# Optimization experiments

Measured on AMD Instinct MI355X. Metric: run time of the kernel, lower is better.

Reference implementation:

```python
import jax, jax.numpy as jnp
import numpy as np

N = 100000
E = 1000000
D_IN = 64
H1, C1 = 12, 12   # conv1: heads=12, out=12 -> concat 144
H2, C2 = 1, 64    # conv2: heads=1, out=64
NEG_SLOPE = 0.2
ALPHA = 0.5       # SSGConv alpha, K=1


def setup_inputs() -> dict:
    key = jax.random.key(0)
    ks = jax.random.split(key, 16)
    features = jax.random.normal(ks[0], (N, D_IN), dtype=jnp.float32)
    # edges with no self loops (PyG GATv2 removes then re-adds self loops)
    src = jax.random.randint(ks[1], (E,), 0, N)
    off = jax.random.randint(ks[2], (E,), 1, N)
    dst = (src + off) % N
    edge_index = jnp.stack([src, dst]).astype(jnp.int64)
    g = lambda k, shape, fan: (jax.random.normal(k, shape, jnp.float32) * (1.0 / np.sqrt(fan)))
    params = dict(
        W_ssg=g(ks[3], (D_IN, D_IN), D_IN), b_ssg=jnp.zeros((D_IN,), jnp.float32),
        W1l=g(ks[4], (D_IN, H1 * C1), D_IN), b1l=jnp.zeros((H1 * C1,), jnp.float32),
        W1r=g(ks[5], (D_IN, H1 * C1), D_IN), b1r=jnp.zeros((H1 * C1,), jnp.float32),
        att1=g(ks[6], (H1, C1), C1), bias1=jnp.zeros((H1 * C1,), jnp.float32),
        W2l=g(ks[7], (H1 * C1, H2 * C2), H1 * C1), b2l=jnp.zeros((H2 * C2,), jnp.float32),
        W2r=g(ks[8], (H1 * C1, H2 * C2), H1 * C1), b2r=jnp.zeros((H2 * C2,), jnp.float32),
        att2=g(ks[9], (H2, C2), C2), bias2=jnp.zeros((H2 * C2,), jnp.float32),
    )
    return dict(features=features, edge_index=edge_index, **params)


def _add_self_loops(src, dst):
    loop = jnp.arange(N, dtype=src.dtype)
    return jnp.concatenate([src, loop]), jnp.concatenate([dst, loop])


def _ssg_conv(x, src, dst, W, b):
    # gcn_norm with self loops, edge weight 1
    s, d = _add_self_loops(src, dst)
    deg = jax.ops.segment_sum(jnp.ones_like(s, dtype=x.dtype), d, num_segments=N)
    dinv = jnp.where(deg > 0, jax.lax.rsqrt(deg), 0.0)
    norm = dinv[s] * dinv[d]                      # [E+N]
    agg = jax.ops.segment_sum(x[s] * norm[:, None], d, num_segments=N)
    h = ALPHA * x + (1.0 - ALPHA) * agg           # K=1
    return h @ W + b


def _gatv2_conv(x, src, dst, Wl, bl, Wr, br, att, bias, Hh, Cc):
    s, d = _add_self_loops(src, dst)
    xl = (x @ Wl + bl).reshape(N, Hh, Cc)
    xr = (x @ Wr + br).reshape(N, Hh, Cc)
    e = jax.nn.leaky_relu(xl[s] + xr[d], NEG_SLOPE)       # [E', H, C]
    logits = jnp.einsum('ehc,hc->eh', e, att)             # [E', H]
    m = jax.ops.segment_max(logits, d, num_segments=N)    # [N, H]
    a = jnp.exp(logits - m[d])
    denom = jax.ops.segment_sum(a, d, num_segments=N)
    a = a / (denom[d] + 1e-16)                            # segment softmax
    out = jax.ops.segment_sum(xl[s] * a[:, :, None], d, num_segments=N)
    return out.reshape(N, Hh * Cc) + bias


def reference(features, edge_index, W_ssg, b_ssg, W1l, b1l, W1r, b1r,
              att1, bias1, W2l, b2l, W2r, b2r, att2, bias2):
    src, dst = edge_index[0], edge_index[1]
    x = _ssg_conv(features, src, dst, W_ssg, b_ssg)
    x = _gatv2_conv(x, src, dst, W1l, b1l, W1r, b1r, att1, bias1, H1, C1)
    x = _gatv2_conv(x, src, dst, W2l, b2l, W2r, b2r, att2, bias2, H2, C2)
    return x
```

## Files before the change

kernel.cpp:

```cpp
#include <hip/hip_runtime.h>

#define NNODE 100000
#define NEDGE 1000000
#define CAP 64

typedef __attribute__((ext_vector_type(4))) float f32x4;
typedef __attribute__((ext_vector_type(8))) short bf16x8;

__device__ __forceinline__ float lrelu(float x){ return x >= 0.f ? x : 0.2f*x; }
__device__ __forceinline__ unsigned short f2bf(float f){
    unsigned u = __float_as_uint(f);
    unsigned r = (u + 0x7FFFu + ((u >> 16) & 1u)) >> 16;
    return (unsigned short)r;
}
__device__ __forceinline__ float bf2f(unsigned short h){
    return __uint_as_float(((unsigned)h) << 16);
}

__global__ void detect_kernel(const int* __restrict__ ei, int* __restrict__ flag){
    if (threadIdx.x == 0 && blockIdx.x == 0){
        int nz = 0;
        for (int i = 1; i < 64; i += 2) nz |= ei[i];
        flag[0] = (nz == 0) ? 1 : 0;
    }
}

__global__ __launch_bounds__(256) void scatter_kernel(const int* __restrict__ ei,
                                                      const int* __restrict__ flag,
                                                      int* __restrict__ cnt,
                                                      int* __restrict__ col){
    int e = blockIdx.x * 256 + threadIdx.x;
    if (e >= NEDGE) return;
    int s, d;
    if (flag[0]){ s = ei[2*e]; d = ei[2*(NEDGE + e)]; }
    else        { s = ei[e];   d = ei[NEDGE + e]; }
    if ((unsigned)s < NNODE && (unsigned)d < NNODE){
        int p = atomicAdd(&cnt[d], 1);
        if (p < CAP) col[d*CAP + p] = s;
    }
}

__global__ __launch_bounds__(256) void dinv_kernel(const int* __restrict__ cnt,
                                                   float* __restrict__ dinv){
    int i = blockIdx.x * 256 + threadIdx.x;
    if (i < NNODE) dinv[i] = rsqrtf((float)(cnt[i] + 1));
}

__global__ __launch_bounds__(256) void foldw_kernel(const float* __restrict__ Wssg,
                                                    const float* __restrict__ bssg,
                                                    const float* __restrict__ W1l,
                                                    const float* __restrict__ b1l,
                                                    const float* __restrict__ W1r,
                                                    const float* __restrict__ b1r,
                                                    unsigned short* __restrict__ Wct,
                                                    float* __restrict__ bc){
    int id = blockIdx.x * 256 + threadIdx.x;
    if (id < 2*64*144){
        int which = id / (64*144);
        int rem = id - which*64*144;
        int k = rem / 144, j = rem - (rem/144)*144;
        const float* W1 = which ? W1r : W1l;
        float s = 0.f;
        #pragma unroll 8
        for (int c = 0; c < 64; ++c)
            s = fmaf(Wssg[k*64 + c], W1[c*144 + j], s);
        Wct[(size_t)(which*144 + j)*64 + k] = f2bf(s);
    }
    if (id < 2*144){
        int which = id / 144, j = id - which*144;
        const float* W1 = which ? W1r : W1l;
        const float* b1 = which ? b1r : b1l;
        float s = b1[j];
        #pragma unroll 8
        for (int c = 0; c < 64; ++c)
            s = fmaf(bssg[c], W1[c*144 + j], s);
        bc[which*144 + j] = s;
    }
}

__global__ __launch_bounds__(256) void castw2_kernel(const float* __restrict__ W2l,
                                                     const float* __restrict__ b2l,
                                                     const float* __restrict__ W2r,
                                                     const float* __restrict__ b2r,
                                                     unsigned short* __restrict__ W2t,
                                                     float* __restrict__ b2c){
    int id = blockIdx.x * 256 + threadIdx.x;
    if (id < 128*160){
        int j = id / 160, k = id - (id/160)*160;
        float v = 0.f;
        if (k < 144) v = (j < 64) ? W2l[k*64 + j] : W2r[k*64 + (j - 64)];
        W2t[(size_t)j*160 + k] = f2bf(v);
    }
    if (id < 128) b2c[id] = (id < 64) ? b2l[id] : b2r[id - 64];
}

__global__ __launch_bounds__(256) void ssg_kernel(const float* __restrict__ x,
                                                  const int* __restrict__ col,
                                                  const int* __restrict__ cnt,
                                                  const float* __restrict__ dinv,
                                                  unsigned short* __restrict__ hb){
    int wid = threadIdx.x >> 6, lane = threadIdx.x & 63;
    int d = blockIdx.x * 4 + wid;
    int cq = lane & 15, eq = lane >> 4;
    float di = dinv[d];
    int deg = min(cnt[d], CAP);
    int myc = (lane < deg) ? col[d*CAP + lane] : 0;
    float wl = (lane < deg) ? dinv[myc] : 0.f;
    float a0 = 0.f, a1 = 0.f, a2 = 0.f, a3 = 0.f;
    for (int e0 = 0; e0 < deg; e0 += 4){
        int e = e0 + eq;
        bool val = e < deg;
        int idx = val ? e : 0;
        int se = __shfl(myc, idx);
        float w = __shfl(wl, idx);
        if (!val) w = 0.f;
        float4 v = *(const float4*)&x[(size_t)se*64 + 4*cq];
        a0 = fmaf(w, v.x, a0);
        a1 = fmaf(w, v.y, a1);
        a2 = fmaf(w, v.z, a2);
        a3 = fmaf(w, v.w, a3);
    }
    #pragma unroll
    for (int m = 16; m < 64; m <<= 1){
        a0 += __shfl_xor(a0, m);
        a1 += __shfl_xor(a1, m);
        a2 += __shfl_xor(a2, m);
        a3 += __shfl_xor(a3, m);
    }
    if (eq == 0){
        float4 xd = *(const float4*)&x[(size_t)d*64 + 4*cq];
        float dd = di*di;
        ushort4 o;
        o.x = f2bf(0.5f*xd.x + 0.5f*fmaf(di, a0, dd*xd.x));
        o.y = f2bf(0.5f*xd.y + 0.5f*fmaf(di, a1, dd*xd.y));
        o.z = f2bf(0.5f*xd.z + 0.5f*fmaf(di, a2, dd*xd.z));
        o.w = f2bf(0.5f*xd.w + 0.5f*fmaf(di, a3, dd*xd.w));
        *(ushort4*)&hb[(size_t)d*64 + 4*cq] = o;
    }
}

template<int K, int OUT1, int OUT2>
__global__ __launch_bounds__(256) void gemm_mfma_kernel(const unsigned short* __restrict__ Xb,
                                                        const unsigned short* __restrict__ Wt,
                                                        const float* __restrict__ Bc,
                                                        unsigned short* __restrict__ Y1,
                                                        unsigned short* __restrict__ Y2){
    constexpr int OUT = OUT1 + OUT2;
    constexpr int NT = OUT / 16;
    int wid = threadIdx.x >> 6, lane = threadIdx.x & 63;
    int m = lane & 15, kg = lane >> 4;
    int row0 = blockIdx.x * 64 + wid * 16;
    int rA = row0 + m; if (rA > NNODE-1) rA = NNODE-1;
    f32x4 acc[NT];
    #pragma unroll
    for (int t = 0; t < NT; ++t) acc[t] = (f32x4){0.f, 0.f, 0.f, 0.f};
    #pragma unroll
    for (int k0 = 0; k0 < K; k0 += 32){
        bf16x8 a = *(const bf16x8*)&Xb[(size_t)rA*K + k0 + 8*kg];
        #pragma unroll
        for (int t = 0; t < NT; ++t){
            bf16x8 b = *(const bf16x8*)&Wt[(size_t)(t*16 + m)*K + k0 + 8*kg];
            acc[t] = __builtin_amdgcn_mfma_f32_16x16x32_bf16(a, b, acc[t], 0, 0, 0);
        }
    }
    int rbase = row0 + 4*kg;
    #pragma unroll
    for (int t = 0; t < NT; ++t){
        int colg = t*16 + m;
        float bias = Bc[colg];
        #pragma unroll
        for (int r = 0; r < 4; ++r){
            int gr = rbase + r;
            if (gr < NNODE){
                unsigned short v = f2bf(acc[t][r] + bias);
                if (colg < OUT1) Y1[(size_t)gr*OUT1 + colg] = v;
                else             Y2[(size_t)gr*OUT2 + (colg - OUT1)] = v;
            }
        }
    }
}

__global__ __launch_bounds__(192) void gat1_kernel(const unsigned short* __restrict__ xl,
                                                   const unsigned short* __restrict__ xr,
                                                   const int* __restrict__ col,
                                                   const int* __restrict__ cnt,
                                                   const float* __restrict__ att,
                                                   const float* __restrict__ bias,
                                                   unsigned short* __restrict__ xg){
    __shared__ __align__(16) float V[16][148];
    __shared__ float A[16][13];
    __shared__ int scol[65];
    int d = blockIdx.x, t = threadIdx.x;
    int deg = min(cnt[d], CAP);
    int ne = deg + 1;
    if (t < deg) scol[t] = col[d*CAP + t];
    if (t == deg) scol[t] = d;
    int h = t % 12;
    int eslot = t / 12;
    float xrr[12], attr[12];
    {
        const ushort4* xrp = (const ushort4*)&xr[(size_t)d*144 + h*12];
        ushort4 q0 = xrp[0], q1 = xrp[1], q2 = xrp[2];
        xrr[0]=bf2f(q0.x); xrr[1]=bf2f(q0.y); xrr[2]=bf2f(q0.z); xrr[3]=bf2f(q0.w);
        xrr[4]=bf2f(q1.x); xrr[5]=bf2f(q1.y); xrr[6]=bf2f(q1.z); xrr[7]=bf2f(q1.w);
        xrr[8]=bf2f(q2.x); xrr[9]=bf2f(q2.y); xrr[10]=bf2f(q2.z); xrr[11]=bf2f(q2.w);
    }
    #pragma unroll
    for (int c = 0; c < 12; ++c) attr[c] = att[h*12 + c];
    int hh = t / 12;
    float acc = 0.f, l = 0.f;
    __syncthreads();
    for (int e0 = 0; e0 < ne; e0 += 16){
        int e = e0 + eslot;
        if (e < ne){
            const ushort4* row = (const ushort4*)&xl[(size_t)scol[e]*144 + h*12];
            ushort4 q0 = row[0], q1 = row[1], q2 = row[2];
            float v0=bf2f(q0.x), v1=bf2f(q0.y), v2=bf2f(q0.z), v3=bf2f(q0.w);
            float v4=bf2f(q1.x), v5=bf2f(q1.y), v6=bf2f(q1.z), v7=bf2f(q1.w);
            float v8=bf2f(q2.x), v9=bf2f(q2.y), v10=bf2f(q2.z), v11=bf2f(q2.w);
            float s = 0.f;
            s = fmaf(lrelu(v0 + xrr[0]),  attr[0],  s);
            s = fmaf(lrelu(v1 + xrr[1]),  attr[1],  s);
            s = fmaf(lrelu(v2 + xrr[2]),  attr[2],  s);
            s = fmaf(lrelu(v3 + xrr[3]),  attr[3],  s);
            s = fmaf(lrelu(v4 + xrr[4]),  attr[4],  s);
            s = fmaf(lrelu(v5 + xrr[5]),  attr[5],  s);
            s = fmaf(lrelu(v6 + xrr[6]),  attr[6],  s);
            s = fmaf(lrelu(v7 + xrr[7]),  attr[7],  s);
            s = fmaf(lrelu(v8 + xrr[8]),  attr[8],  s);
            s = fmaf(lrelu(v9 + xrr[9]),  attr[9],  s);
            s = fmaf(lrelu(v10 + xrr[10]), attr[10], s);
            s = fmaf(lrelu(v11 + xrr[11]), attr[11], s);
            A[eslot][h] = __expf(s);
            float4 f0 = make_float4(v0, v1, v2, v3);
            float4 f1 = make_float4(v4, v5, v6, v7);
            float4 f2 = make_float4(v8, v9, v10, v11);
            *(float4*)&V[eslot][h*12]     = f0;
            *(float4*)&V[eslot][h*12 + 4] = f1;
            *(float4*)&V[eslot][h*12 + 8] = f2;
        }
        __syncthreads();
        if (t < 144){
            int lim = ne - e0; if (lim > 16) lim = 16;
            for (int ee = 0; ee < lim; ++ee){
                float a  = A[ee][hh];
                float xv = V[ee][t];
                l += a;
                acc = fmaf(a, xv, acc);
            }
        }
        __syncthreads();
    }
    if (t < 144) xg[(size_t)d*160 + t] = f2bf(acc / (l + 1e-16f) + bias[t]);
    else if (t < 160) xg[(size_t)d*160 + t] = 0;
}

__global__ __launch_bounds__(256) void gat2_kernel(const unsigned short* __restrict__ xl,
                                                   const unsigned short* __restrict__ xr,
                                                   const int* __restrict__ col,
                                                   const int* __restrict__ cnt,
                                                   const float* __restrict__ att,
                                                   const float* __restrict__ bias,
                                                   float* __restrict__ out){
    __shared__ float V[4][8][68];
    __shared__ float Aw[4][8];
    int wid = threadIdx.x >> 6, lane = threadIdx.x & 63;
    int d0 = blockIdx.x * 4;
    int d = d0 + wid;
    int deg = min(cnt[d], 63);
    int ne = deg + 1;
    int nemax = 1;
    #pragma unroll
    for (int j = 0; j < 4; ++j) nemax = max(nemax, min(cnt[d0+j], 63) + 1);
    int eq = lane >> 3, cq = lane & 7;
    float4 xra, xrb;
    {
        ushort4 u0 = *(const ushort4*)&xr[(size_t)d*64 + 8*cq];
        ushort4 u1 = *(const ushort4*)&xr[(size_t)d*64 + 8*cq + 4];
        xra = make_float4(bf2f(u0.x), bf2f(u0.y), bf2f(u0.z), bf2f(u0.w));
        xrb = make_float4(bf2f(u1.x), bf2f(u1.y), bf2f(u1.z), bf2f(u1.w));
    }
    float4 ata = *(const float4*)&att[8*cq];
    float4 atb = *(const float4*)&att[8*cq + 4];
    int myc = (lane < deg) ? col[d*CAP + lane] : d;
    float acc = 0.f, l = 0.f;
    for (int e0 = 0; e0 < nemax; e0 += 8){
        int e = e0 + eq;
        bool val = (e < ne);
        int se = __shfl(myc, val ? e : 0);
        float4 va = make_float4(0.f,0.f,0.f,0.f), vb = va;
        if (val){
            ushort4 u0 = *(const ushort4*)&xl[(size_t)se*64 + 8*cq];
            ushort4 u1 = *(const ushort4*)&xl[(size_t)se*64 + 8*cq + 4];
            va = make_float4(bf2f(u0.x), bf2f(u0.y), bf2f(u0.z), bf2f(u0.w));
            vb = make_float4(bf2f(u1.x), bf2f(u1.y), bf2f(u1.z), bf2f(u1.w));
        }
        float part = 0.f;
        part = fmaf(lrelu(va.x + xra.x), ata.x, part);
        part = fmaf(lrelu(va.y + xra.y), ata.y, part);
        part = fmaf(lrelu(va.z + xra.z), ata.z, part);
        part = fmaf(lrelu(va.w + xra.w), ata.w, part);
        part = fmaf(lrelu(vb.x + xrb.x), atb.x, part);
        part = fmaf(lrelu(vb.y + xrb.y), atb.y, part);
        part = fmaf(lrelu(vb.z + xrb.z), atb.z, part);
        part = fmaf(lrelu(vb.w + xrb.w), atb.w, part);
        part += __shfl_xor(part, 1);
        part += __shfl_xor(part, 2);
        part += __shfl_xor(part, 4);
        *(float4*)&V[wid][eq][8*cq]     = va;
        *(float4*)&V[wid][eq][8*cq + 4] = vb;
        if (cq == 0) Aw[wid][eq] = val ? __expf(part) : 0.f;
        __syncthreads();
        int lim = ne - e0; if (lim > 8) lim = 8;
        for (int j = 0; j < lim; ++j){
            float a = Aw[wid][j];
            l += a;
            acc = fmaf(a, V[wid][j][lane], acc);
        }
        __syncthreads();
    }
    out[(size_t)d*64 + lane] = acc / (l + 1e-16f) + bias[lane];
}

extern "C" void kernel_launch(void* const* d_in, const int* in_sizes, int n_in,
                              void* d_out, int out_size, void* d_ws, size_t ws_size,
                              hipStream_t stream){
    const float* feat  = (const float*)d_in[0];
    const int*   ei    = (const int*)d_in[1];
    const float* W_ssg = (const float*)d_in[2];
    const float* b_ssg = (const float*)d_in[3];
    const float* W1l   = (const float*)d_in[4];
    const float* b1l   = (const float*)d_in[5];
    const float* W1r   = (const float*)d_in[6];
    const float* b1r   = (const float*)d_in[7];
    const float* att1  = (const float*)d_in[8];
    const float* bias1 = (const float*)d_in[9];
    const float* W2l   = (const float*)d_in[10];
    const float* b2l   = (const float*)d_in[11];
    const float* W2r   = (const float*)d_in[12];
    const float* b2r   = (const float*)d_in[13];
    const float* att2  = (const float*)d_in[14];
    const float* bias2 = (const float*)d_in[15];
    float* out = (float*)d_out;

    char* ws = (char*)d_ws;
    size_t off = 0;
    auto alloc = [&](size_t bytes)->void*{
        void* p = ws + off; off = (off + bytes + 255) & ~(size_t)255; return p;
    };
    int*            flag = (int*)           alloc(4);
    int*            cnt  = (int*)           alloc((size_t)NNODE*4);
    int*            col  = (int*)           alloc((size_t)NNODE*CAP*4);
    float*          dinv = (float*)         alloc((size_t)NNODE*4);
    unsigned short* hb   = (unsigned short*)alloc((size_t)NNODE*64*2);
    unsigned short* xl1b = (unsigned short*)alloc((size_t)NNODE*144*2);
    unsigned short* xr1b = (unsigned short*)alloc((size_t)NNODE*144*2);
    unsigned short* xg   = (unsigned short*)alloc((size_t)NNODE*160*2);
    unsigned short* xl2b = (unsigned short*)alloc((size_t)NNODE*64*2);
    unsigned short* xr2b = (unsigned short*)alloc((size_t)NNODE*64*2);
    unsigned short* Wct  = (unsigned short*)alloc((size_t)288*64*2);
    float*          bc   = (float*)         alloc((size_t)288*4);
    unsigned short* W2t  = (unsigned short*)alloc((size_t)128*160*2);
    float*          b2c  = (float*)         alloc((size_t)128*4);

    hipMemsetAsync(cnt, 0, (size_t)NNODE*4, stream);
    detect_kernel<<<1, 64, 0, stream>>>(ei, flag);
    scatter_kernel<<<(NEDGE + 255)/256, 256, 0, stream>>>(ei, flag, cnt, col);
    dinv_kernel<<<(NNODE + 255)/256, 256, 0, stream>>>(cnt, dinv);
    foldw_kernel<<<72, 256, 0, stream>>>(W_ssg, b_ssg, W1l, b1l, W1r, b1r, Wct, bc);
    castw2_kernel<<<80, 256, 0, stream>>>(W2l, b2l, W2r, b2r, W2t, b2c);

    ssg_kernel<<<NNODE/4, 256, 0, stream>>>(feat, col, cnt, dinv, hb);

    gemm_mfma_kernel<64,144,144><<<1563, 256, 0, stream>>>(hb, Wct, bc, xl1b, xr1b);

    gat1_kernel<<<NNODE, 192, 0, stream>>>(xl1b, xr1b, col, cnt, att1, bias1, xg);

    gemm_mfma_kernel<160,64,64><<<1563, 256, 0, stream>>>(xg, W2t, b2c, xl2b, xr2b);

    gat2_kernel<<<NNODE/4, 256, 0, stream>>>(xl2b, xr2b, col, cnt, att2, bias2, out);
}
```

Baseline: 493.5 us.

## Merge setup kernels, widen ssg loads, and vectorize gat1 aggregation

Combines the dinv, weight-fold and W2 cast kernels into a single launch to cut launch overhead, and turns the flag detection into one parallel ballot. The ssg kernel now gives each lane 8 channels with two float4 loads, so 8 edges are processed per wavefront step. The gat1 aggregation splits edges across 4 groups, with float4 channel reads from shared memory, and adds a cross-group reduction through shared memory. These trade extra shared memory and a sync for more parallel accumulation and fewer launches.

```diff
diff --git a/kernel.cpp b/kernel.cpp
--- a/kernel.cpp
+++ b/kernel.cpp
@@ -18,11 +18,10 @@
 }
 
 __global__ void detect_kernel(const int* __restrict__ ei, int* __restrict__ flag){
-    if (threadIdx.x == 0 && blockIdx.x == 0){
-        int nz = 0;
-        for (int i = 1; i < 64; i += 2) nz |= ei[i];
-        flag[0] = (nz == 0) ? 1 : 0;
-    }
+    int t = threadIdx.x;
+    int nz = ei[2*t + 1];
+    unsigned long long b = __ballot(nz != 0);
+    if (t == 0) flag[0] = (b == 0ULL) ? 1 : 0;
 }
 
 __global__ __launch_bounds__(256) void scatter_kernel(const int* __restrict__ ei,
@@ -40,58 +39,59 @@
     }
 }
 
-__global__ __launch_bounds__(256) void dinv_kernel(const int* __restrict__ cnt,
-                                                   float* __restrict__ dinv){
-    int i = blockIdx.x * 256 + threadIdx.x;
-    if (i < NNODE) dinv[i] = rsqrtf((float)(cnt[i] + 1));
-}
-
-__global__ __launch_bounds__(256) void foldw_kernel(const float* __restrict__ Wssg,
+__global__ __launch_bounds__(256) void setup_kernel(const int* __restrict__ cnt,
+                                                    float* __restrict__ dinv,
+                                                    const float* __restrict__ Wssg,
                                                     const float* __restrict__ bssg,
                                                     const float* __restrict__ W1l,
                                                     const float* __restrict__ b1l,
                                                     const float* __restrict__ W1r,
                                                     const float* __restrict__ b1r,
                                                     unsigned short* __restrict__ Wct,
-                                                    float* __restrict__ bc){
-    int id = blockIdx.x * 256 + threadIdx.x;
-    if (id < 2*64*144){
-        int which = id / (64*144);
-        int rem = id - which*64*144;
-        int k = rem / 144, j = rem - (rem/144)*144;
-        const float* W1 = which ? W1r : W1l;
-        float s = 0.f;
-        #pragma unroll 8
-        for (int c = 0; c < 64; ++c)
-            s = fmaf(Wssg[k*64 + c], W1[c*144 + j], s);
-        Wct[(size_t)(which*144 + j)*64 + k] = f2bf(s);
-    }
-    if (id < 2*144){
-        int which = id / 144, j = id - which*144;
-        const float* W1 = which ? W1r : W1l;
-        const float* b1 = which ? b1r : b1l;
-        float s = b1[j];
-        #pragma unroll 8
-        for (int c = 0; c < 64; ++c)
-            s = fmaf(bssg[c], W1[c*144 + j], s);
-        bc[which*144 + j] = s;
-    }
-}
-
-__global__ __launch_bounds__(256) void castw2_kernel(const float* __restrict__ W2l,
-                                                     const float* __restrict__ b2l,
-                                                     const float* __restrict__ W2r,
-                                                     const float* __restrict__ b2r,
-                                                     unsigned short* __restrict__ W2t,
-                                                     float* __restrict__ b2c){
-    int id = blockIdx.x * 256 + threadIdx.x;
-    if (id < 128*160){
-        int j = id / 160, k = id - (id/160)*160;
-        float v = 0.f;
-        if (k < 144) v = (j < 64) ? W2l[k*64 + j] : W2r[k*64 + (j - 64)];
-        W2t[(size_t)j*160 + k] = f2bf(v);
-    }
-    if (id < 128) b2c[id] = (id < 64) ? b2l[id] : b2r[id - 64];
+                                                    float* __restrict__ bc,
+                                                    const float* __restrict__ W2l,
+                                                    const float* __restrict__ b2l,
+                                                    const float* __restrict__ W2r,
+                                                    const float* __restrict__ b2r,
+                                                    unsigned short* __restrict__ W2t,
+                                                    float* __restrict__ b2c){
+    int b = blockIdx.x;
+    if (b < 391){
+        int i = b * 256 + threadIdx.x;
+        if (i < NNODE) dinv[i] = rsqrtf((float)(cnt[i] + 1));
+    } else if (b < 463){
+        int id = (b - 391) * 256 + threadIdx.x;
+        if (id < 2*64*144){
+            int which = id / (64*144);
+            int rem = id - which*64*144;
+            int k = rem / 144, j = rem - (rem/144)*144;
+            const float* W1 = which ? W1r : W1l;
+            float s = 0.f;
+            #pragma unroll 8
+            for (int c = 0; c < 64; ++c)
+                s = fmaf(Wssg[k*64 + c], W1[c*144 + j], s);
+            Wct[(size_t)(which*144 + j)*64 + k] = f2bf(s);
+        }
+        if (id < 2*144){
+            int which = id / 144, j = id - which*144;
+            const float* W1 = which ? W1r : W1l;
+            const float* b1 = which ? b1r : b1l;
+            float s = b1[j];
+            #pragma unroll 8
+            for (int c = 0; c < 64; ++c)
+                s = fmaf(bssg[c], W1[c*144 + j], s);
+            bc[which*144 + j] = s;
+        }
+    } else {
+        int id = (b - 463) * 256 + threadIdx.x;
+        if (id < 128*160){
+            int j = id / 160, k = id - (id/160)*160;
+            float v = 0.f;
+            if (k < 144) v = (j < 64) ? W2l[k*64 + j] : W2r[k*64 + (j - 64)];
+            W2t[(size_t)j*160 + k] = f2bf(v);
+        }
+        if (id < 128) b2c[id] = (id < 64) ? b2l[id] : b2r[id - 64];
+    }
 }
 
 __global__ __launch_bounds__(256) void ssg_kernel(const float* __restrict__ x,
@@ -101,41 +101,48 @@
                                                   unsigned short* __restrict__ hb){
     int wid = threadIdx.x >> 6, lane = threadIdx.x & 63;
     int d = blockIdx.x * 4 + wid;
-    int cq = lane & 15, eq = lane >> 4;
+    int cq = lane & 7, eq = lane >> 3;
     float di = dinv[d];
     int deg = min(cnt[d], CAP);
     int myc = (lane < deg) ? col[d*CAP + lane] : 0;
     float wl = (lane < deg) ? dinv[myc] : 0.f;
-    float a0 = 0.f, a1 = 0.f, a2 = 0.f, a3 = 0.f;
-    for (int e0 = 0; e0 < deg; e0 += 4){
+    float a0=0.f,a1=0.f,a2=0.f,a3=0.f,a4=0.f,a5=0.f,a6=0.f,a7=0.f;
+    for (int e0 = 0; e0 < deg; e0 += 8){
         int e = e0 + eq;
         bool val = e < deg;
         int idx = val ? e : 0;
         int se = __shfl(myc, idx);
         float w = __shfl(wl, idx);
         if (!val) w = 0.f;
-        float4 v = *(const float4*)&x[(size_t)se*64 + 4*cq];
-        a0 = fmaf(w, v.x, a0);
-        a1 = fmaf(w, v.y, a1);
-        a2 = fmaf(w, v.z, a2);
-        a3 = fmaf(w, v.w, a3);
-    }
-    #pragma unroll
-    for (int m = 16; m < 64; m <<= 1){
-        a0 += __shfl_xor(a0, m);
-        a1 += __shfl_xor(a1, m);
-        a2 += __shfl_xor(a2, m);
-        a3 += __shfl_xor(a3, m);
+        float4 v0 = *(const float4*)&x[(size_t)se*64 + 8*cq];
+        float4 v1 = *(const float4*)&x[(size_t)se*64 + 8*cq + 4];
+        a0 = fmaf(w, v0.x, a0); a1 = fmaf(w, v0.y, a1);
+        a2 = fmaf(w, v0.z, a2); a3 = fmaf(w, v0.w, a3);
+        a4 = fmaf(w, v1.x, a4); a5 = fmaf(w, v1.y, a5);
+        a6 = fmaf(w, v1.z, a6); a7 = fmaf(w, v1.w, a7);
+    }
+    #pragma unroll
+    for (int m = 8; m < 64; m <<= 1){
+        a0 += __shfl_xor(a0, m); a1 += __shfl_xor(a1, m);
+        a2 += __shfl_xor(a2, m); a3 += __shfl_xor(a3, m);
+        a4 += __shfl_xor(a4, m); a5 += __shfl_xor(a5, m);
+        a6 += __shfl_xor(a6, m); a7 += __shfl_xor(a7, m);
     }
     if (eq == 0){
-        float4 xd = *(const float4*)&x[(size_t)d*64 + 4*cq];
+        float4 xd0 = *(const float4*)&x[(size_t)d*64 + 8*cq];
+        float4 xd1 = *(const float4*)&x[(size_t)d*64 + 8*cq + 4];
         float dd = di*di;
-        ushort4 o;
-        o.x = f2bf(0.5f*xd.x + 0.5f*fmaf(di, a0, dd*xd.x));
-        o.y = f2bf(0.5f*xd.y + 0.5f*fmaf(di, a1, dd*xd.y));
-        o.z = f2bf(0.5f*xd.z + 0.5f*fmaf(di, a2, dd*xd.z));
-        o.w = f2bf(0.5f*xd.w + 0.5f*fmaf(di, a3, dd*xd.w));
-        *(ushort4*)&hb[(size_t)d*64 + 4*cq] = o;
+        ushort4 o0, o1;
+        o0.x = f2bf(0.5f*xd0.x + 0.5f*fmaf(di, a0, dd*xd0.x));
+        o0.y = f2bf(0.5f*xd0.y + 0.5f*fmaf(di, a1, dd*xd0.y));
+        o0.z = f2bf(0.5f*xd0.z + 0.5f*fmaf(di, a2, dd*xd0.z));
+        o0.w = f2bf(0.5f*xd0.w + 0.5f*fmaf(di, a3, dd*xd0.w));
+        o1.x = f2bf(0.5f*xd1.x + 0.5f*fmaf(di, a4, dd*xd1.x));
+        o1.y = f2bf(0.5f*xd1.y + 0.5f*fmaf(di, a5, dd*xd1.y));
+        o1.z = f2bf(0.5f*xd1.z + 0.5f*fmaf(di, a6, dd*xd1.z));
+        o1.w = f2bf(0.5f*xd1.w + 0.5f*fmaf(di, a7, dd*xd1.w));
+        *(ushort4*)&hb[(size_t)d*64 + 8*cq]     = o0;
+        *(ushort4*)&hb[(size_t)d*64 + 8*cq + 4] = o1;
     }
 }
 
@@ -189,6 +196,8 @@
                                                    unsigned short* __restrict__ xg){
     __shared__ __align__(16) float V[16][148];
     __shared__ float A[16][13];
+    __shared__ __align__(16) float P[4][36][4];
+    __shared__ float Lp[4][12];
     __shared__ int scol[65];
     int d = blockIdx.x, t = threadIdx.x;
     int deg = min(cnt[d], CAP);
@@ -207,8 +216,10 @@
     }
     #pragma unroll
     for (int c = 0; c < 12; ++c) attr[c] = att[h*12 + c];
-    int hh = t / 12;
-    float acc = 0.f, l = 0.f;
+    int eg = t / 36, cg = t - (t/36)*36;
+    int hc = cg / 3;
+    float4 acc4 = make_float4(0.f, 0.f, 0.f, 0.f);
+    float l = 0.f;
     __syncthreads();
     for (int e0 = 0; e0 < ne; e0 += 16){
         int e = e0 + eslot;
@@ -232,27 +243,38 @@
             s = fmaf(lrelu(v10 + xrr[10]), attr[10], s);
             s = fmaf(lrelu(v11 + xrr[11]), attr[11], s);
             A[eslot][h] = __expf(s);
-            float4 f0 = make_float4(v0, v1, v2, v3);
-            float4 f1 = make_float4(v4, v5, v6, v7);
-            float4 f2 = make_float4(v8, v9, v10, v11);
-            *(float4*)&V[eslot][h*12]     = f0;
-            *(float4*)&V[eslot][h*12 + 4] = f1;
-            *(float4*)&V[eslot][h*12 + 8] = f2;
+            *(float4*)&V[eslot][h*12]     = make_float4(v0, v1, v2, v3);
+            *(float4*)&V[eslot][h*12 + 4] = make_float4(v4, v5, v6, v7);
+            *(float4*)&V[eslot][h*12 + 8] = make_float4(v8, v9, v10, v11);
         }
         __syncthreads();
         if (t < 144){
             int lim = ne - e0; if (lim > 16) lim = 16;
-            for (int ee = 0; ee < lim; ++ee){
-                float a  = A[ee][hh];
-                float xv = V[ee][t];
+            for (int ee = eg; ee < lim; ee += 4){
+                float a = A[ee][hc];
+                float4 v = *(const float4*)&V[ee][4*cg];
+                acc4.x = fmaf(a, v.x, acc4.x);
+                acc4.y = fmaf(a, v.y, acc4.y);
+                acc4.z = fmaf(a, v.z, acc4.z);
+                acc4.w = fmaf(a, v.w, acc4.w);
                 l += a;
-                acc = fmaf(a, xv, acc);
             }
         }
         __syncthreads();
     }
-    if (t < 144) xg[(size_t)d*160 + t] = f2bf(acc / (l + 1e-16f) + bias[t]);
-    else if (t < 160) xg[(size_t)d*160 + t] = 0;
+    if (t < 144){
+        *(float4*)&P[eg][cg][0] = acc4;
+        if (cg - hc*3 == 0) Lp[eg][hc] = l;
+    }
+    __syncthreads();
+    if (t < 144){
+        int cgf = t >> 2, cif = t & 3, hh = t / 12;
+        float acc = P[0][cgf][cif] + P[1][cgf][cif] + P[2][cgf][cif] + P[3][cgf][cif];
+        float ll  = Lp[0][hh] + Lp[1][hh] + Lp[2][hh] + Lp[3][hh];
+        xg[(size_t)d*160 + t] = f2bf(acc / (ll + 1e-16f) + bias[t]);
+    } else if (t < 160){
+        xg[(size_t)d*160 + t] = 0;
+    }
 }
 
 __global__ __launch_bounds__(256) void gat2_kernel(const unsigned short* __restrict__ xl,
@@ -366,9 +388,9 @@
     hipMemsetAsync(cnt, 0, (size_t)NNODE*4, stream);
     detect_kernel<<<1, 64, 0, stream>>>(ei, flag);
     scatter_kernel<<<(NEDGE + 255)/256, 256, 0, stream>>>(ei, flag, cnt, col);
-    dinv_kernel<<<(NNODE + 255)/256, 256, 0, stream>>>(cnt, dinv);
-    foldw_kernel<<<72, 256, 0, stream>>>(W_ssg, b_ssg, W1l, b1l, W1r, b1r, Wct, bc);
-    castw2_kernel<<<80, 256, 0, stream>>>(W2l, b2l, W2r, b2r, W2t, b2c);
+    setup_kernel<<<543, 256, 0, stream>>>(cnt, dinv,
+                                          W_ssg, b_ssg, W1l, b1l, W1r, b1r, Wct, bc,
+                                          W2l, b2l, W2r, b2r, W2t, b2c);
 
     ssg_kernel<<<NNODE/4, 256, 0, stream>>>(feat, col, cnt, dinv, hb);
 
```

New measurement: 495.7 us. Within noise of the previous version (+0.4%).
